# Optimization experiments

Hardware: AMD Instinct MI355X
Metric: run time of the kernel (lower is better)

The kernel has to match this reference:

```python
import jax, jax.numpy as jnp
import numpy as np

N_NODES = 50000
N_EDGES = 800000
N_PRED = 100000  # pos and neg each
D_IN = 256
D_HID = 128  # hard-coded hidden width of conv1
D_OUT = 128  # out_channels


def _lin_params(key, fan_in, fan_out, dtype=jnp.float32):
    kw, kb = jax.random.split(key)
    s = 1.0 / np.sqrt(fan_in)
    W = jax.random.uniform(kw, (fan_in, fan_out), dtype, -s, s)
    b = jax.random.uniform(kb, (fan_out,), dtype, -s, s)
    return W, b


def setup_inputs() -> dict:
    key = jax.random.key(0)
    ks = jax.random.split(key, 16)
    inp = {
        "x": jax.random.normal(ks[0], (N_NODES, D_IN), jnp.float32),
        "edge_index": jax.random.randint(ks[1], (2, N_EDGES), 0, N_NODES, jnp.int64),
        "pos_edge_index": jax.random.randint(ks[2], (2, N_PRED), 0, N_NODES, jnp.int64),
        "neg_edge_index": jax.random.randint(ks[3], (2, N_PRED), 0, N_NODES, jnp.int64),
    }
    # conv1: TransformerConv(D_IN -> D_HID), heads=1, root_weight=True
    inp["Wq1"], inp["bq1"] = _lin_params(ks[4], D_IN, D_HID)
    inp["Wk1"], inp["bk1"] = _lin_params(ks[5], D_IN, D_HID)
    inp["Wv1"], inp["bv1"] = _lin_params(ks[6], D_IN, D_HID)
    inp["Ws1"], inp["bs1"] = _lin_params(ks[7], D_IN, D_HID)
    # conv2: TransformerConv(D_HID -> D_OUT)
    inp["Wq2"], inp["bq2"] = _lin_params(ks[8], D_HID, D_OUT)
    inp["Wk2"], inp["bk2"] = _lin_params(ks[9], D_HID, D_OUT)
    inp["Wv2"], inp["bv2"] = _lin_params(ks[10], D_HID, D_OUT)
    inp["Ws2"], inp["bs2"] = _lin_params(ks[11], D_HID, D_OUT)
    # final edge scorer Linear(D_OUT, 1)
    inp["Wl"], inp["bl"] = _lin_params(ks[12], D_OUT, 1)
    return inp


def _transformer_conv(x, Wq, bq, Wk, bk, Wv, bv, Ws, bs, src, dst, n_nodes):
    # PyG TransformerConv, heads=1, concat=True, root_weight=True, no edge attrs.
    C = Wq.shape[1]
    q = x @ Wq + bq  # [N, C] queries (destination side)
    k = x @ Wk + bk  # [N, C] keys (source side)
    v = x @ Wv + bv  # [N, C] values (source side)
    # per-edge attention logits, softmax normalized over incoming edges of dst
    alpha = jnp.einsum("ec,ec->e", q[dst], k[src]) / jnp.sqrt(jnp.asarray(C, x.dtype))
    amax = jax.lax.stop_gradient(jax.ops.segment_max(alpha, dst, num_segments=n_nodes))
    ex = jnp.exp(alpha - amax[dst])
    den = jax.ops.segment_sum(ex, dst, num_segments=n_nodes)
    w = ex / den[dst]  # [E]
    agg = jax.ops.segment_sum(v[src] * w[:, None], dst, num_segments=n_nodes)  # [N, C]
    return agg + (x @ Ws + bs)  # skip connection (lin_skip)


def reference(x, edge_index, pos_edge_index, neg_edge_index,
              Wq1, bq1, Wk1, bk1, Wv1, bv1, Ws1, bs1,
              Wq2, bq2, Wk2, bk2, Wv2, bv2, Ws2, bs2,
              Wl, bl):
    src, dst = edge_index[0], edge_index[1]
    h = _transformer_conv(x, Wq1, bq1, Wk1, bk1, Wv1, bv1, Ws1, bs1, src, dst, N_NODES)
    h = jax.nn.relu(h)
    h = _transformer_conv(h, Wq2, bq2, Wk2, bk2, Wv2, bv2, Ws2, bs2, src, dst, N_NODES)
    ei = jnp.concatenate([pos_edge_index, neg_edge_index], axis=-1)  # [2, 2*N_PRED]
    prod = h[ei[0]] * h[ei[1]]  # [2*N_PRED, D_OUT]
    return (prod @ Wl + bl).squeeze(-1)  # [2*N_PRED]
```

## Files before the change

### kernel.cpp

```cpp
#include <hip/hip_runtime.h>
#include <cstdint>
#include <cstddef>

#define NN 50000
#define NE 800000
#define NP 100000
#define NB 196

typedef _Float16 h8v __attribute__((ext_vector_type(8)));
typedef _Float16 h4v __attribute__((ext_vector_type(4)));
typedef float    f4v __attribute__((ext_vector_type(4)));

#define ATTN_SCALE 0.088388347648318447f

__device__ inline void load_lds16(const void* gptr, void* ldsptr) {
  __builtin_amdgcn_global_load_lds(
      (const __attribute__((address_space(1))) void*)gptr,
      (__attribute__((address_space(3))) void*)ldsptr, 16, 0, 0);
}

__global__ __launch_bounds__(256) void hist_kernel(const int* __restrict__ dst,
                                                   int* __restrict__ deg,
                                                   int* __restrict__ rank, int E) {
  int e = blockIdx.x * 256 + threadIdx.x;
  if (e < E) rank[e] = atomicAdd(&deg[dst[e]], 1);
}

__global__ __launch_bounds__(256) void scan1_kernel(const int* __restrict__ deg,
                                                    int* __restrict__ loc,
                                                    int* __restrict__ bsum, int n) {
  __shared__ int sh[256];
  int tid = threadIdx.x;
  int i = blockIdx.x * 256 + tid;
  int val = (i < n) ? deg[i] : 0;
  sh[tid] = val;
  __syncthreads();
  for (int off = 1; off < 256; off <<= 1) {
    int add = (tid >= off) ? sh[tid - off] : 0;
    __syncthreads();
    sh[tid] += add;
    __syncthreads();
  }
  if (i < n) loc[i] = sh[tid] - val;
  if (tid == 255) bsum[blockIdx.x] = sh[255];
}

__global__ __launch_bounds__(256) void scan2_kernel(int* __restrict__ bsum, int nb) {
  __shared__ int sh[256];
  int tid = threadIdx.x;
  int v = (tid < nb) ? bsum[tid] : 0;
  sh[tid] = v;
  __syncthreads();
  for (int off = 1; off < 256; off <<= 1) {
    int add = (tid >= off) ? sh[tid - off] : 0;
    __syncthreads();
    sh[tid] += add;
    __syncthreads();
  }
  if (tid < nb) bsum[tid] = sh[tid] - v;
}

__global__ __launch_bounds__(256) void scan3_kernel(const int* __restrict__ loc,
                                                    const int* __restrict__ bsum,
                                                    int* __restrict__ offs, int n, int E) {
  int i = blockIdx.x * 256 + threadIdx.x;
  if (i < n) offs[i] = loc[i] + bsum[blockIdx.x];
  if (i == 0) offs[n] = E;
}

__global__ __launch_bounds__(256) void scatter_kernel(const int* __restrict__ src,
                                                      const int* __restrict__ dst,
                                                      const int* __restrict__ offs,
                                                      const int* __restrict__ rank,
                                                      int* __restrict__ csr_src, int E) {
  int e = blockIdx.x * 256 + threadIdx.x;
  if (e < E) {
    int d = dst[e];
    csr_src[offs[d] + rank[e]] = src[e];
  }
}

__global__ __launch_bounds__(256) void cvt_f16_kernel(const float* __restrict__ X,
                                                      _Float16* __restrict__ Xf, int n4) {
  int i = blockIdx.x * 256 + threadIdx.x;
  if (i >= n4) return;
  float4 x = ((const float4*)X)[i];
  h4v o = {(_Float16)x.x, (_Float16)x.y, (_Float16)x.z, (_Float16)x.w};
  ((h4v*)Xf)[i] = o;
}

__global__ __launch_bounds__(256) void packw_kernel(
    const float* __restrict__ Wq1, const float* __restrict__ Wk1,
    const float* __restrict__ Wv1, const float* __restrict__ Ws1,
    const float* __restrict__ Wq2, const float* __restrict__ Wk2,
    const float* __restrict__ Wv2, const float* __restrict__ Ws2,
    _Float16* __restrict__ WT1, _Float16* __restrict__ WT2) {
  int b = blockIdx.x;
  int k = threadIdx.x;
  if (b < 512) {
    int n = b;
    const float* W;
    switch (n >> 7) {
      case 0:  W = Wq1; break;
      case 1:  W = Wk1; break;
      case 2:  W = Wv1; break;
      default: W = Ws1; break;
    }
    WT1[(size_t)n * 256 + k] = (_Float16)W[(size_t)k * 128 + (n & 127)];
  } else if (k < 128) {
    int n = b - 512;
    const float* W;
    switch (n >> 7) {
      case 0:  W = Wq2; break;
      case 1:  W = Wk2; break;
      case 2:  W = Wv2; break;
      default: W = Ws2; break;
    }
    WT2[(size_t)n * 128 + k] = (_Float16)W[(size_t)k * 128 + (n & 127)];
  }
}

__global__ __launch_bounds__(512) void gemm_all_kernel(
    const _Float16* __restrict__ A, int M, int K,
    const _Float16* __restrict__ BT,
    const float* __restrict__ bq, const float* __restrict__ bk,
    const float* __restrict__ bv, const float* __restrict__ bs,
    _Float16* __restrict__ Oq, _Float16* __restrict__ Okv,
    _Float16* __restrict__ Os) {
  __shared__ _Float16 As[128 * 64];
  __shared__ _Float16 Bs[512 * 64];

  const int tx = threadIdx.x;
  const int w = tx >> 6;
  const int lane = tx & 63;
  const int lr = lane & 15;
  const int q = lane >> 4;
  const int wm = w >> 2;
  const int wn = w & 3;
  const int row0 = blockIdx.x * 128;

  f4v acc[4][8];
#pragma unroll
  for (int i = 0; i < 4; ++i)
#pragma unroll
    for (int j = 0; j < 8; ++j) acc[i][j] = (f4v){0.f, 0.f, 0.f, 0.f};

  for (int k0 = 0; k0 < K; k0 += 64) {
    __syncthreads();
#pragma unroll
    for (int o = 0; o < 2; ++o) {
      int i = o * 8 + w;
      int r = i * 8 + (lane >> 3);
      int cl = (lane & 7) ^ (r & 7);
      int gr = row0 + r;
      if (gr > M - 1) gr = M - 1;
      load_lds16(A + (size_t)gr * K + k0 + cl * 8, &As[i * 8 * 64]);
    }
#pragma unroll
    for (int o = 0; o < 8; ++o) {
      int i = o * 8 + w;
      int r = i * 8 + (lane >> 3);
      int cl = (lane & 7) ^ (r & 7);
      load_lds16(BT + (size_t)r * K + k0 + cl * 8, &Bs[i * 8 * 64]);
    }
    __syncthreads();

#pragma unroll
    for (int kk = 0; kk < 2; ++kk) {
      h8v af[4], bf[8];
#pragma unroll
      for (int t = 0; t < 4; ++t) {
        int row = wm * 64 + t * 16 + lr;
        af[t] = *(const h8v*)&As[row * 64 + (((kk * 4 + q) ^ (row & 7)) * 8)];
      }
#pragma unroll
      for (int u = 0; u < 8; ++u) {
        int col = wn * 128 + u * 16 + lr;
        bf[u] = *(const h8v*)&Bs[col * 64 + (((kk * 4 + q) ^ (col & 7)) * 8)];
      }
#pragma unroll
      for (int mt = 0; mt < 4; ++mt)
#pragma unroll
        for (int nt = 0; nt < 8; ++nt)
          acc[mt][nt] = __builtin_amdgcn_mfma_f32_16x16x32_f16(af[mt], bf[nt],
                                                               acc[mt][nt], 0, 0, 0);
    }
  }

  const float* bp = (wn == 0) ? bq : (wn == 1) ? bk : (wn == 2) ? bv : bs;
#pragma unroll
  for (int half = 0; half < 2; ++half) {
    __syncthreads();
    if (wm == half) {
#pragma unroll
      for (int nt = 0; nt < 8; ++nt) {
        int col = wn * 128 + nt * 16 + lr;
        float bval = bp[nt * 16 + lr];
#pragma unroll
        for (int mt = 0; mt < 4; ++mt)
#pragma unroll
          for (int reg = 0; reg < 4; ++reg) {
            int r = mt * 16 + q * 4 + reg;
            Bs[r * 512 + col] = (_Float16)(acc[mt][nt][reg] + bval);
          }
      }
    }
    __syncthreads();
#pragma unroll
    for (int i = 0; i < 8; ++i) {
      int sl = i * 512 + tx;
      int rr = sl >> 6;
      int c8 = sl & 63;
      int col = c8 * 8;
      int grow = row0 + half * 64 + rr;
      if (grow < M) {
        int p = c8 >> 4;
        int cp = col & 127;
        _Float16* dst;
        switch (p) {
          case 0:  dst = Oq  + (size_t)grow * 128 + cp;       break;
          case 1:  dst = Okv + (size_t)grow * 256 + cp;       break;
          case 2:  dst = Okv + (size_t)grow * 256 + 128 + cp; break;
          default: dst = Os  + (size_t)grow * 128 + cp;       break;
        }
        *(h8v*)dst = *(const h8v*)&Bs[rr * 512 + col];
      }
    }
  }
}

__global__ __launch_bounds__(256) void attn_fused_kernel(
    const _Float16* __restrict__ qf, const _Float16* __restrict__ kvf,
    const _Float16* __restrict__ sf,
    const int* __restrict__ offs, const int* __restrict__ csr_src,
    _Float16* __restrict__ hf, int n_nodes, int do_relu) {
  int node = (int)((blockIdx.x * 256u + threadIdx.x) >> 6);
  if (node >= n_nodes) return;
  int lane = threadIdx.x & 63;
  int g = lane >> 4;
  int t = lane & 15;

  h8v qv = *(const h8v*)(qf + (size_t)node * 128 + t * 8);
  int beg = offs[node], end = offs[node + 1];

  float den = 0.f;
  float acc[8];
#pragma unroll
  for (int j = 0; j < 8; ++j) acc[j] = 0.f;

  int e = beg + g;
  for (; e + 12 < end; e += 16) {
    int sn0 = csr_src[e];
    int sn1 = csr_src[e + 4];
    int sn2 = csr_src[e + 8];
    int sn3 = csr_src[e + 12];
    const _Float16* r0 = kvf + (size_t)sn0 * 256 + t * 8;
    const _Float16* r1 = kvf + (size_t)sn1 * 256 + t * 8;
    const _Float16* r2 = kvf + (size_t)sn2 * 256 + t * 8;
    const _Float16* r3 = kvf + (size_t)sn3 * 256 + t * 8;
    h8v k0 = *(const h8v*)r0, v0 = *(const h8v*)(r0 + 128);
    h8v k1 = *(const h8v*)r1, v1 = *(const h8v*)(r1 + 128);
    h8v k2 = *(const h8v*)r2, v2 = *(const h8v*)(r2 + 128);
    h8v k3 = *(const h8v*)r3, v3 = *(const h8v*)(r3 + 128);
    float p0 = 0.f, p1 = 0.f, p2 = 0.f, p3 = 0.f;
#pragma unroll
    for (int j = 0; j < 8; ++j) {
      p0 = fmaf((float)qv[j], (float)k0[j], p0);
      p1 = fmaf((float)qv[j], (float)k1[j], p1);
      p2 = fmaf((float)qv[j], (float)k2[j], p2);
      p3 = fmaf((float)qv[j], (float)k3[j], p3);
    }
#pragma unroll
    for (int o = 1; o < 16; o <<= 1) {
      p0 += __shfl_xor(p0, o);
      p1 += __shfl_xor(p1, o);
      p2 += __shfl_xor(p2, o);
      p3 += __shfl_xor(p3, o);
    }
    float w0 = __expf(p0 * ATTN_SCALE);
    float w1 = __expf(p1 * ATTN_SCALE);
    float w2 = __expf(p2 * ATTN_SCALE);
    float w3 = __expf(p3 * ATTN_SCALE);
    den += (w0 + w1) + (w2 + w3);
#pragma unroll
    for (int j = 0; j < 8; ++j) {
      acc[j] = fmaf(w0, (float)v0[j], acc[j]);
      acc[j] = fmaf(w1, (float)v1[j], acc[j]);
      acc[j] = fmaf(w2, (float)v2[j], acc[j]);
      acc[j] = fmaf(w3, (float)v3[j], acc[j]);
    }
  }
  for (; e < end; e += 4) {
    int sn0 = csr_src[e];
    const _Float16* r0 = kvf + (size_t)sn0 * 256 + t * 8;
    h8v k0 = *(const h8v*)r0, v0 = *(const h8v*)(r0 + 128);
    float p0 = 0.f;
#pragma unroll
    for (int j = 0; j < 8; ++j) p0 = fmaf((float)qv[j], (float)k0[j], p0);
#pragma unroll
    for (int o = 1; o < 16; o <<= 1) p0 += __shfl_xor(p0, o);
    float w0 = __expf(p0 * ATTN_SCALE);
    den += w0;
#pragma unroll
    for (int j = 0; j < 8; ++j) acc[j] = fmaf(w0, (float)v0[j], acc[j]);
  }

#pragma unroll
  for (int j = 0; j < 8; ++j) {
    acc[j] += __shfl_xor(acc[j], 16);
    acc[j] += __shfl_xor(acc[j], 32);
  }
  den += __shfl_xor(den, 16);
  den += __shfl_xor(den, 32);

  if (g == 0) {
    float inv = (end > beg) ? 1.f / den : 0.f;
    h8v sk = *(const h8v*)(sf + (size_t)node * 128 + t * 8);
    h8v of;
#pragma unroll
    for (int j = 0; j < 8; ++j) {
      float o = fmaf(acc[j], inv, (float)sk[j]);
      if (do_relu) o = fmaxf(o, 0.f);
      of[j] = (_Float16)o;
    }
    *(h8v*)(hf + (size_t)node * 128 + t * 8) = of;
  }
}

__global__ __launch_bounds__(256) void scorer_kernel(
    const _Float16* __restrict__ hf,
    const int* __restrict__ pos0, const int* __restrict__ pos1,
    const int* __restrict__ neg0, const int* __restrict__ neg1,
    const float* __restrict__ Wl, const float* __restrict__ bl,
    float* __restrict__ out, int npred) {
  int eid = (int)((blockIdx.x * 256u + threadIdx.x) >> 4);
  if (eid >= 2 * npred) return;
  int t = threadIdx.x & 15;

  int a, b;
  if (eid < npred) { a = pos0[eid]; b = pos1[eid]; }
  else             { a = neg0[eid - npred]; b = neg1[eid - npred]; }

  h8v ha = *(const h8v*)(hf + (size_t)a * 128 + t * 8);
  h8v hb = *(const h8v*)(hf + (size_t)b * 128 + t * 8);
  const float4* wp = (const float4*)(Wl + t * 8);
  float4 w0 = wp[0], w1 = wp[1];
  float wl[8] = {w0.x, w0.y, w0.z, w0.w, w1.x, w1.y, w1.z, w1.w};
  float p = 0.f;
#pragma unroll
  for (int j = 0; j < 8; ++j)
    p = fmaf((float)ha[j] * (float)hb[j], wl[j], p);
  p += __shfl_xor(p, 1);
  p += __shfl_xor(p, 2);
  p += __shfl_xor(p, 4);
  p += __shfl_xor(p, 8);
  if (t == 0) out[eid] = p + bl[0];
}

extern "C" void kernel_launch(void* const* d_in, const int* in_sizes, int n_in,
                              void* d_out, int out_size, void* d_ws, size_t ws_size,
                              hipStream_t stream) {
  const float* x   = (const float*)d_in[0];
  const int*   ei  = (const int*)d_in[1];
  const int*   pos = (const int*)d_in[2];
  const int*   neg = (const int*)d_in[3];
  const float* Wq1 = (const float*)d_in[4];  const float* bq1 = (const float*)d_in[5];
  const float* Wk1 = (const float*)d_in[6];  const float* bk1 = (const float*)d_in[7];
  const float* Wv1 = (const float*)d_in[8];  const float* bv1 = (const float*)d_in[9];
  const float* Ws1 = (const float*)d_in[10]; const float* bs1 = (const float*)d_in[11];
  const float* Wq2 = (const float*)d_in[12]; const float* bq2 = (const float*)d_in[13];
  const float* Wk2 = (const float*)d_in[14]; const float* bk2 = (const float*)d_in[15];
  const float* Wv2 = (const float*)d_in[16]; const float* bv2 = (const float*)d_in[17];
  const float* Ws2 = (const float*)d_in[18]; const float* bs2 = (const float*)d_in[19];
  const float* Wl  = (const float*)d_in[20]; const float* bl  = (const float*)d_in[21];
  float* out = (float*)d_out;

  const size_t NODE_C = (size_t)NN * 128;
  char* p = (char*)d_ws;
  _Float16* qf  = (_Float16*)p; p += NODE_C * 2;
  _Float16* kvf = (_Float16*)p; p += NODE_C * 4;
  _Float16* sf  = (_Float16*)p; p += NODE_C * 2;
  _Float16* h1  = (_Float16*)p; p += NODE_C * 2;
  _Float16* h2  = (_Float16*)p; p += NODE_C * 2;
  _Float16* Xf  = (_Float16*)p; p += (size_t)NN * 256 * 2;
  _Float16* WT1 = (_Float16*)p; p += 512 * 256 * 2;
  _Float16* WT2 = (_Float16*)p; p += 512 * 128 * 2;
  int* rank    = (int*)p;      p += (size_t)NE * 4;
  int* deg     = (int*)p;      p += (size_t)NN * 4;
  int* loc     = (int*)p;      p += (size_t)NN * 4;
  int* bsum    = (int*)p;      p += 256 * 4;
  int* offs    = (int*)p;      p += (size_t)(NN + 8) * 4;
  int* csr_src = (int*)p;      p += (size_t)NE * 4;

  const int* e_src = ei;
  const int* e_dst = ei + NE;

  hipMemsetAsync(deg, 0, NN * sizeof(int), stream);
  hist_kernel<<<(NE + 255) / 256, 256, 0, stream>>>(e_dst, deg, rank, NE);
  scan1_kernel<<<NB, 256, 0, stream>>>(deg, loc, bsum, NN);
  scan2_kernel<<<1, 256, 0, stream>>>(bsum, NB);
  scan3_kernel<<<NB, 256, 0, stream>>>(loc, bsum, offs, NN, NE);
  scatter_kernel<<<(NE + 255) / 256, 256, 0, stream>>>(e_src, e_dst, offs, rank,
                                                       csr_src, NE);

  cvt_f16_kernel<<<(NN * 256 / 4 + 255) / 256, 256, 0, stream>>>(x, Xf, NN * 256 / 4);
  packw_kernel<<<1024, 256, 0, stream>>>(Wq1, Wk1, Wv1, Ws1, Wq2, Wk2, Wv2, Ws2,
                                         WT1, WT2);

  int ggrid = (NN + 127) / 128;
  int attn_blocks = (NN * 64 + 255) / 256;

  gemm_all_kernel<<<ggrid, 512, 0, stream>>>(Xf, NN, 256, WT1,
                                             bq1, bk1, bv1, bs1, qf, kvf, sf);
  attn_fused_kernel<<<attn_blocks, 256, 0, stream>>>(
      qf, kvf, sf, offs, csr_src, h1, NN, 1);

  gemm_all_kernel<<<ggrid, 512, 0, stream>>>(h1, NN, 128, WT2,
                                             bq2, bk2, bv2, bs2, qf, kvf, sf);
  attn_fused_kernel<<<attn_blocks, 256, 0, stream>>>(
      qf, kvf, sf, offs, csr_src, h2, NN, 0);

  scorer_kernel<<<(2 * NP * 16 + 255) / 256, 256, 0, stream>>>(
      h2, pos, pos + NP, neg, neg + NP, Wl, bl, out, NP);
}
```

Before: 383.8 us.

## Merge prep kernels, fuse scan stages, use 16-bit CSR indices and fdot2 attention

```diff
diff --git a/kernel.cpp b/kernel.cpp
--- a/kernel.cpp
+++ b/kernel.cpp
@@ -7,8 +7,13 @@
 #define NP 100000
 #define NB 196
 
+#define CVT_BLOCKS   12500
+#define PACKW_BLOCKS 1024
+#define HIST_BLOCKS  3125
+
 typedef _Float16 h8v __attribute__((ext_vector_type(8)));
 typedef _Float16 h4v __attribute__((ext_vector_type(4)));
+typedef _Float16 h2v __attribute__((ext_vector_type(2)));
 typedef float    f4v __attribute__((ext_vector_type(4)));
 
 #define ATTN_SCALE 0.088388347648318447f
@@ -19,11 +24,64 @@
       (__attribute__((address_space(3))) void*)ldsptr, 16, 0, 0);
 }
 
-__global__ __launch_bounds__(256) void hist_kernel(const int* __restrict__ dst,
-                                                   int* __restrict__ deg,
-                                                   int* __restrict__ rank, int E) {
-  int e = blockIdx.x * 256 + threadIdx.x;
-  if (e < E) rank[e] = atomicAdd(&deg[dst[e]], 1);
+__device__ inline float dot8(h8v a, h8v b, float c) {
+  union U { h8v v; h2v p[4]; };
+  U ua; ua.v = a;
+  U ub; ub.v = b;
+#if __has_builtin(__builtin_amdgcn_fdot2)
+  c = __builtin_amdgcn_fdot2(ua.p[0], ub.p[0], c, false);
+  c = __builtin_amdgcn_fdot2(ua.p[1], ub.p[1], c, false);
+  c = __builtin_amdgcn_fdot2(ua.p[2], ub.p[2], c, false);
+  c = __builtin_amdgcn_fdot2(ua.p[3], ub.p[3], c, false);
+#else
+#pragma unroll
+  for (int j = 0; j < 8; ++j) c = fmaf((float)a[j], (float)b[j], c);
+#endif
+  return c;
+}
+
+__global__ __launch_bounds__(256) void prep_kernel(
+    const float* __restrict__ x, _Float16* __restrict__ Xf,
+    const float* __restrict__ Wq1, const float* __restrict__ Wk1,
+    const float* __restrict__ Wv1, const float* __restrict__ Ws1,
+    const float* __restrict__ Wq2, const float* __restrict__ Wk2,
+    const float* __restrict__ Wv2, const float* __restrict__ Ws2,
+    _Float16* __restrict__ WT1, _Float16* __restrict__ WT2,
+    const int* __restrict__ dst, int* __restrict__ deg, int* __restrict__ rank) {
+  int b = blockIdx.x;
+  int tid = threadIdx.x;
+  if (b < CVT_BLOCKS) {
+    int i = b * 256 + tid;
+    float4 xv = ((const float4*)x)[i];
+    h4v o = {(_Float16)xv.x, (_Float16)xv.y, (_Float16)xv.z, (_Float16)xv.w};
+    ((h4v*)Xf)[i] = o;
+  } else if (b < CVT_BLOCKS + PACKW_BLOCKS) {
+    int bb = b - CVT_BLOCKS;
+    if (bb < 512) {
+      int n = bb;
+      const float* W;
+      switch (n >> 7) {
+        case 0:  W = Wq1; break;
+        case 1:  W = Wk1; break;
+        case 2:  W = Wv1; break;
+        default: W = Ws1; break;
+      }
+      WT1[(size_t)n * 256 + tid] = (_Float16)W[(size_t)tid * 128 + (n & 127)];
+    } else if (tid < 128) {
+      int n = bb - 512;
+      const float* W;
+      switch (n >> 7) {
+        case 0:  W = Wq2; break;
+        case 1:  W = Wk2; break;
+        case 2:  W = Wv2; break;
+        default: W = Ws2; break;
+      }
+      WT2[(size_t)n * 128 + tid] = (_Float16)W[(size_t)tid * 128 + (n & 127)];
+    }
+  } else {
+    int e = (b - CVT_BLOCKS - PACKW_BLOCKS) * 256 + tid;
+    if (e < NE) rank[e] = atomicAdd(&deg[dst[e]], 1);
+  }
 }
 
 __global__ __launch_bounds__(256) void scan1_kernel(const int* __restrict__ deg,
@@ -45,78 +103,36 @@
   if (tid == 255) bsum[blockIdx.x] = sh[255];
 }
 
-__global__ __launch_bounds__(256) void scan2_kernel(int* __restrict__ bsum, int nb) {
+__global__ __launch_bounds__(256) void scan23_kernel(const int* __restrict__ loc,
+                                                     const int* __restrict__ bsum,
+                                                     int* __restrict__ offs,
+                                                     int n, int E) {
   __shared__ int sh[256];
-  int tid = threadIdx.x;
-  int v = (tid < nb) ? bsum[tid] : 0;
-  sh[tid] = v;
+  int bid = blockIdx.x, tid = threadIdx.x;
+  int pre = 0;
+  for (int j = tid; j < bid; j += 256) pre += bsum[j];
+  sh[tid] = pre;
   __syncthreads();
-  for (int off = 1; off < 256; off <<= 1) {
-    int add = (tid >= off) ? sh[tid - off] : 0;
-    __syncthreads();
-    sh[tid] += add;
-    __syncthreads();
-  }
-  if (tid < nb) bsum[tid] = sh[tid] - v;
-}
-
-__global__ __launch_bounds__(256) void scan3_kernel(const int* __restrict__ loc,
-                                                    const int* __restrict__ bsum,
-                                                    int* __restrict__ offs, int n, int E) {
-  int i = blockIdx.x * 256 + threadIdx.x;
-  if (i < n) offs[i] = loc[i] + bsum[blockIdx.x];
-  if (i == 0) offs[n] = E;
+  for (int off = 128; off > 0; off >>= 1) {
+    if (tid < off) sh[tid] += sh[tid + off];
+    __syncthreads();
+  }
+  int base = sh[0];
+  int i = bid * 256 + tid;
+  if (i < n) offs[i] = loc[i] + base;
+  if (bid == 0 && tid == 0) offs[n] = E;
 }
 
 __global__ __launch_bounds__(256) void scatter_kernel(const int* __restrict__ src,
                                                       const int* __restrict__ dst,
                                                       const int* __restrict__ offs,
                                                       const int* __restrict__ rank,
-                                                      int* __restrict__ csr_src, int E) {
+                                                      unsigned short* __restrict__ csr_src,
+                                                      int E) {
   int e = blockIdx.x * 256 + threadIdx.x;
   if (e < E) {
     int d = dst[e];
-    csr_src[offs[d] + rank[e]] = src[e];
-  }
-}
-
-__global__ __launch_bounds__(256) void cvt_f16_kernel(const float* __restrict__ X,
-                                                      _Float16* __restrict__ Xf, int n4) {
-  int i = blockIdx.x * 256 + threadIdx.x;
-  if (i >= n4) return;
-  float4 x = ((const float4*)X)[i];
-  h4v o = {(_Float16)x.x, (_Float16)x.y, (_Float16)x.z, (_Float16)x.w};
-  ((h4v*)Xf)[i] = o;
-}
-
-__global__ __launch_bounds__(256) void packw_kernel(
-    const float* __restrict__ Wq1, const float* __restrict__ Wk1,
-    const float* __restrict__ Wv1, const float* __restrict__ Ws1,
-    const float* __restrict__ Wq2, const float* __restrict__ Wk2,
-    const float* __restrict__ Wv2, const float* __restrict__ Ws2,
-    _Float16* __restrict__ WT1, _Float16* __restrict__ WT2) {
-  int b = blockIdx.x;
-  int k = threadIdx.x;
-  if (b < 512) {
-    int n = b;
-    const float* W;
-    switch (n >> 7) {
-      case 0:  W = Wq1; break;
-      case 1:  W = Wk1; break;
-      case 2:  W = Wv1; break;
-      default: W = Ws1; break;
-    }
-    WT1[(size_t)n * 256 + k] = (_Float16)W[(size_t)k * 128 + (n & 127)];
-  } else if (k < 128) {
-    int n = b - 512;
-    const float* W;
-    switch (n >> 7) {
-      case 0:  W = Wq2; break;
-      case 1:  W = Wk2; break;
-      case 2:  W = Wv2; break;
-      default: W = Ws2; break;
-    }
-    WT2[(size_t)n * 128 + k] = (_Float16)W[(size_t)k * 128 + (n & 127)];
+    csr_src[offs[d] + rank[e]] = (unsigned short)src[e];
   }
 }
 
@@ -216,14 +232,14 @@
       if (grow < M) {
         int p = c8 >> 4;
         int cp = col & 127;
-        _Float16* dst;
+        _Float16* dstp;
         switch (p) {
-          case 0:  dst = Oq  + (size_t)grow * 128 + cp;       break;
-          case 1:  dst = Okv + (size_t)grow * 256 + cp;       break;
-          case 2:  dst = Okv + (size_t)grow * 256 + 128 + cp; break;
-          default: dst = Os  + (size_t)grow * 128 + cp;       break;
+          case 0:  dstp = Oq  + (size_t)grow * 128 + cp;       break;
+          case 1:  dstp = Okv + (size_t)grow * 256 + cp;       break;
+          case 2:  dstp = Okv + (size_t)grow * 256 + 128 + cp; break;
+          default: dstp = Os  + (size_t)grow * 128 + cp;       break;
         }
-        *(h8v*)dst = *(const h8v*)&Bs[rr * 512 + col];
+        *(h8v*)dstp = *(const h8v*)&Bs[rr * 512 + col];
       }
     }
   }
@@ -232,7 +248,7 @@
 __global__ __launch_bounds__(256) void attn_fused_kernel(
     const _Float16* __restrict__ qf, const _Float16* __restrict__ kvf,
     const _Float16* __restrict__ sf,
-    const int* __restrict__ offs, const int* __restrict__ csr_src,
+    const int* __restrict__ offs, const unsigned short* __restrict__ csr_src,
     _Float16* __restrict__ hf, int n_nodes, int do_relu) {
   int node = (int)((blockIdx.x * 256u + threadIdx.x) >> 6);
   if (node >= n_nodes) return;
@@ -249,56 +265,37 @@
   for (int j = 0; j < 8; ++j) acc[j] = 0.f;
 
   int e = beg + g;
-  for (; e + 12 < end; e += 16) {
+  for (; e + 4 < end; e += 8) {
     int sn0 = csr_src[e];
     int sn1 = csr_src[e + 4];
-    int sn2 = csr_src[e + 8];
-    int sn3 = csr_src[e + 12];
     const _Float16* r0 = kvf + (size_t)sn0 * 256 + t * 8;
     const _Float16* r1 = kvf + (size_t)sn1 * 256 + t * 8;
-    const _Float16* r2 = kvf + (size_t)sn2 * 256 + t * 8;
-    const _Float16* r3 = kvf + (size_t)sn3 * 256 + t * 8;
     h8v k0 = *(const h8v*)r0, v0 = *(const h8v*)(r0 + 128);
     h8v k1 = *(const h8v*)r1, v1 = *(const h8v*)(r1 + 128);
-    h8v k2 = *(const h8v*)r2, v2 = *(const h8v*)(r2 + 128);
-    h8v k3 = *(const h8v*)r3, v3 = *(const h8v*)(r3 + 128);
-    float p0 = 0.f, p1 = 0.f, p2 = 0.f, p3 = 0.f;
-#pragma unroll
-    for (int j = 0; j < 8; ++j) {
-      p0 = fmaf((float)qv[j], (float)k0[j], p0);
-      p1 = fmaf((float)qv[j], (float)k1[j], p1);
-      p2 = fmaf((float)qv[j], (float)k2[j], p2);
-      p3 = fmaf((float)qv[j], (float)k3[j], p3);
-    }
-#pragma unroll
-    for (int o = 1; o < 16; o <<= 1) {
-      p0 += __shfl_xor(p0, o);
-      p1 += __shfl_xor(p1, o);
-      p2 += __shfl_xor(p2, o);
-      p3 += __shfl_xor(p3, o);
-    }
+    float p0 = dot8(qv, k0, 0.f);
+    float p1 = dot8(qv, k1, 0.f);
+    p0 += __shfl_xor(p0, 1); p1 += __shfl_xor(p1, 1);
+    p0 += __shfl_xor(p0, 2); p1 += __shfl_xor(p1, 2);
+    p0 += __shfl_xor(p0, 4); p1 += __shfl_xor(p1, 4);
+    p0 += __shfl_xor(p0, 8); p1 += __shfl_xor(p1, 8);
     float w0 = __expf(p0 * ATTN_SCALE);
     float w1 = __expf(p1 * ATTN_SCALE);
-    float w2 = __expf(p2 * ATTN_SCALE);
-    float w3 = __expf(p3 * ATTN_SCALE);
-    den += (w0 + w1) + (w2 + w3);
+    den += w0 + w1;
 #pragma unroll
     for (int j = 0; j < 8; ++j) {
       acc[j] = fmaf(w0, (float)v0[j], acc[j]);
       acc[j] = fmaf(w1, (float)v1[j], acc[j]);
-      acc[j] = fmaf(w2, (float)v2[j], acc[j]);
-      acc[j] = fmaf(w3, (float)v3[j], acc[j]);
-    }
-  }
-  for (; e < end; e += 4) {
+    }
+  }
+  if (e < end) {
     int sn0 = csr_src[e];
     const _Float16* r0 = kvf + (size_t)sn0 * 256 + t * 8;
     h8v k0 = *(const h8v*)r0, v0 = *(const h8v*)(r0 + 128);
-    float p0 = 0.f;
-#pragma unroll
-    for (int j = 0; j < 8; ++j) p0 = fmaf((float)qv[j], (float)k0[j], p0);
-#pragma unroll
-    for (int o = 1; o < 16; o <<= 1) p0 += __shfl_xor(p0, o);
+    float p0 = dot8(qv, k0, 0.f);
+    p0 += __shfl_xor(p0, 1);
+    p0 += __shfl_xor(p0, 2);
+    p0 += __shfl_xor(p0, 4);
+    p0 += __shfl_xor(p0, 8);
     float w0 = __expf(p0 * ATTN_SCALE);
     den += w0;
 #pragma unroll
@@ -390,22 +387,20 @@
   int* loc     = (int*)p;      p += (size_t)NN * 4;
   int* bsum    = (int*)p;      p += 256 * 4;
   int* offs    = (int*)p;      p += (size_t)(NN + 8) * 4;
-  int* csr_src = (int*)p;      p += (size_t)NE * 4;
+  unsigned short* csr_src = (unsigned short*)p; p += (size_t)NE * 2;
 
   const int* e_src = ei;
   const int* e_dst = ei + NE;
 
   hipMemsetAsync(deg, 0, NN * sizeof(int), stream);
-  hist_kernel<<<(NE + 255) / 256, 256, 0, stream>>>(e_dst, deg, rank, NE);
+
+  prep_kernel<<<CVT_BLOCKS + PACKW_BLOCKS + HIST_BLOCKS, 256, 0, stream>>>(
+      x, Xf, Wq1, Wk1, Wv1, Ws1, Wq2, Wk2, Wv2, Ws2, WT1, WT2, e_dst, deg, rank);
+
   scan1_kernel<<<NB, 256, 0, stream>>>(deg, loc, bsum, NN);
-  scan2_kernel<<<1, 256, 0, stream>>>(bsum, NB);
-  scan3_kernel<<<NB, 256, 0, stream>>>(loc, bsum, offs, NN, NE);
+  scan23_kernel<<<NB, 256, 0, stream>>>(loc, bsum, offs, NN, NE);
   scatter_kernel<<<(NE + 255) / 256, 256, 0, stream>>>(e_src, e_dst, offs, rank,
                                                        csr_src, NE);
-
-  cvt_f16_kernel<<<(NN * 256 / 4 + 255) / 256, 256, 0, stream>>>(x, Xf, NN * 256 / 4);
-  packw_kernel<<<1024, 256, 0, stream>>>(Wq1, Wk1, Wv1, Ws1, Wq2, Wk2, Wv2, Ws2,
-                                         WT1, WT2);
 
   int ggrid = (NN + 127) / 128;
   int attn_blocks = (NN * 64 + 255) / 256;
```

New measurement: 367.5 us. 4.3% less time.
